# Kernel optimization log

Measured on AMD Instinct MI355X. Metric: run time of the kernel, lower is better.

Reference implementation:

```python
import jax, jax.numpy as jnp
import numpy as np

NEG_SLOPE = 0.01  # nn.LeakyReLU default


def setup_inputs() -> dict:
    key = jax.random.key(0)
    k1, k2, k3, k4, k5 = jax.random.split(key, 5)
    SLI, FEAT, NODE = 8, 64, 20000
    N = SLI * NODE          # 160000 graph nodes
    E = 2_560_000           # avg degree 16
    OUT = 64
    inputs = jax.random.normal(k1, (SLI, FEAT, NODE), dtype=jnp.float32)
    src = jax.random.randint(k2, (E,), 0, N, dtype=jnp.int64)
    dst = jax.random.randint(k3, (E,), 0, N, dtype=jnp.int64)
    # GraphConv params (glorot-ish scale)
    W = jax.random.normal(k4, (FEAT, OUT), dtype=jnp.float32) / np.sqrt(FEAT)
    b = jnp.zeros((OUT,), dtype=jnp.float32)
    return {"inputs": inputs, "W": W, "b": b, "src": src, "dst": dst}


def reference(inputs, W, b, src, dst):
    # inputs: [sli, feat, node] -> [sli*node, feat]  (dropout is eval-mode identity)
    sli, feat, node = inputs.shape
    x = jnp.transpose(inputs, (0, 2, 1)).reshape(-1, feat)
    N = sli * node
    ones = jnp.ones(src.shape, dtype=x.dtype)
    deg_out = jax.ops.segment_sum(ones, src, num_segments=N)  # out-degree of src
    deg_in = jax.ops.segment_sum(ones, dst, num_segments=N)   # in-degree of dst
    norm_src = jnp.where(deg_out > 0, deg_out, 1.0) ** -0.5
    norm_dst = jnp.where(deg_in > 0, deg_in, 1.0) ** -0.5
    # norm='both': scale src feats, sum-aggregate over edges, scale dst
    h = x * norm_src[:, None]
    agg = jax.ops.segment_sum(h[src], dst, num_segments=N)    # [N, feat]
    agg = agg * norm_dst[:, None]
    out = agg @ W + b                                          # [N, out]
    out = jax.nn.leaky_relu(out, NEG_SLOPE)
    # [N, out] -> [sli, node, out] -> [sli, out, node]
    return jnp.transpose(out.reshape(sli, node, -1), (0, 2, 1))
```

## Files before the change

### kernel.cpp

```cpp
#include <hip/hip_runtime.h>
#include <hip/hip_bf16.h>

constexpr int SLI  = 8;
constexpr int FEAT = 64;
constexpr int NODE = 20000;
constexpr int NTOT = SLI * NODE;
constexpr int OUTF = 64;
constexpr int CAP  = 48;
constexpr int NB   = 313;
constexpr int BCAP = 8960;
constexpr int EPB  = 4096;
constexpr int NDST = NTOT / 256;

typedef __attribute__((ext_vector_type(8))) short bf16x8;
typedef __attribute__((ext_vector_type(4))) float f32x4;

static __device__ inline unsigned short f2bf(float x) {
    unsigned u = __float_as_uint(x);
    unsigned r = (u + 0x7fffu + ((u >> 16) & 1u)) >> 16;
    return (unsigned short)r;
}

__global__ __launch_bounds__(256) void k_part(const int* __restrict__ src,
                                              const int* __restrict__ dst,
                                              int* __restrict__ cursor_d,
                                              unsigned* __restrict__ bucket_d,
                                              int* __restrict__ cursor_s,
                                              unsigned short* __restrict__ bucket_s, int E) {
    __shared__ unsigned       svalD[EPB];
    __shared__ unsigned short sbktD[EPB];
    __shared__ unsigned       sS[EPB];
    __shared__ int histD[NB], loffD[NB], lcurD[NB], baseD[NB];
    __shared__ int histS[NB], loffS[NB], lcurS[NB], baseS[NB];
    __shared__ int goffD[64], goffS[64];
    int t  = threadIdx.x;
    int e0 = blockIdx.x * EPB;
    for (int i = t; i < NB; i += 256) { histD[i] = 0; histS[i] = 0; }
    __syncthreads();
    int myS[16], myD[16];
#pragma unroll
    for (int i = 0; i < 16; ++i) {
        int idx = e0 + i * 256 + t;
        if (idx < E) {
            myS[i] = src[idx];
            myD[i] = dst[idx];
            atomicAdd(&histD[myD[i] >> 9], 1);
            atomicAdd(&histS[myS[i] >> 9], 1);
        } else { myS[i] = -1; myD[i] = -1; }
    }
    __syncthreads();
    int wv = t >> 6, ln = t & 63;
    if (wv == 0) {
        int b0 = ln * 5, s = 0;
#pragma unroll
        for (int j = 0; j < 5; ++j) { int bb = b0 + j; if (bb < NB) s += histD[bb]; }
        int x = s;
        for (int off = 1; off < 64; off <<= 1) {
            int y = __shfl_up(x, off, 64);
            if (ln >= off) x += y;
        }
        goffD[ln] = x - s;
    } else if (wv == 1) {
        int b0 = ln * 5, s = 0;
#pragma unroll
        for (int j = 0; j < 5; ++j) { int bb = b0 + j; if (bb < NB) s += histS[bb]; }
        int x = s;
        for (int off = 1; off < 64; off <<= 1) {
            int y = __shfl_up(x, off, 64);
            if (ln >= off) x += y;
        }
        goffS[ln] = x - s;
    }
    __syncthreads();
    for (int bb = t; bb < NB; bb += 256) {
        int g5 = bb / 5;
        int sD = goffD[g5], sS2 = goffS[g5];
        for (int k = g5 * 5; k < bb; ++k) { sD += histD[k]; sS2 += histS[k]; }
        loffD[bb] = sD; lcurD[bb] = sD;
        baseD[bb] = atomicAdd(&cursor_d[bb], histD[bb]);
        loffS[bb] = sS2; lcurS[bb] = sS2;
        baseS[bb] = atomicAdd(&cursor_s[bb], histS[bb]);
    }
    __syncthreads();
#pragma unroll
    for (int i = 0; i < 16; ++i) {
        if (myD[i] >= 0) {
            int bD = myD[i] >> 9;
            int p  = atomicAdd(&lcurD[bD], 1);
            svalD[p] = ((unsigned)(myD[i] & 511) << 18) | (unsigned)myS[i];
            sbktD[p] = (unsigned short)bD;
            int bS = myS[i] >> 9;
            int q  = atomicAdd(&lcurS[bS], 1);
            sS[q] = ((unsigned)bS << 9) | (unsigned)(myS[i] & 511);
        }
    }
    __syncthreads();
    int nval = E - e0; if (nval > EPB) nval = EPB;
    for (int p = t; p < nval; p += 256) {
        int bD = sbktD[p];
        int wi = baseD[bD] + (p - loffD[bD]);
        if (wi < BCAP) bucket_d[(size_t)bD * BCAP + wi] = svalD[p];
        unsigned vs = sS[p];
        int bS = vs >> 9;
        int wj = baseS[bS] + (p - loffS[bS]);
        if (wj < BCAP) bucket_s[(size_t)bS * BCAP + wj] = (unsigned short)(vs & 511);
    }
}

__global__ __launch_bounds__(256) void k_fin(const int* __restrict__ cursor_d,
                                             const unsigned* __restrict__ bucket_d,
                                             const int* __restrict__ cursor_s,
                                             const unsigned short* __restrict__ bucket_s,
                                             int* __restrict__ col_ell,
                                             int* __restrict__ deg_in,
                                             int* __restrict__ deg_out) {
    __shared__ char lds[256 * CAP * 4 + 2048];
    int t = threadIdx.x;
    if (blockIdx.x < NDST) {
        int* ell = (int*)lds;
        int* cnt = (int*)(lds + 256 * CAP * 4);
        int blk  = blockIdx.x, b = blk >> 1, half = blk & 1;
        cnt[t] = 0;
        __syncthreads();
        int len = cursor_d[b]; if (len > BCAP) len = BCAP;
        const unsigned* p = bucket_d + (size_t)b * BCAP;
        for (int i = t; i < len; i += 256) {
            unsigned e = p[i];
            int dl = e >> 18;
            if ((dl >> 8) == half) {
                int r = dl & 255;
                int pos = atomicAdd(&cnt[r], 1);
                if (pos < CAP) ell[r * CAP + pos] = (int)(e & 0x3FFFFu);
            }
        }
        __syncthreads();
        int node0 = blk << 8;
        deg_in[node0 + t] = cnt[t];
        size_t gbase = (size_t)node0 * CAP;
        const int4* lsrc = (const int4*)ell;
        int4* gdst = (int4*)(col_ell + gbase);
#pragma unroll
        for (int i = 0; i < 12; ++i)
            gdst[i * 256 + t] = lsrc[i * 256 + t];
    } else {
        int* cnt = (int*)lds;
        int b = blockIdx.x - NDST;
        cnt[t] = 0; cnt[t + 256] = 0;
        __syncthreads();
        int len = cursor_s[b]; if (len > BCAP) len = BCAP;
        const unsigned short* p = bucket_s + (size_t)b * BCAP;
        for (int i = t; i < len; i += 256)
            atomicAdd(&cnt[p[i]], 1);
        __syncthreads();
        int n0 = b << 9;
        if (n0 + t < NTOT)       deg_out[n0 + t] = cnt[t];
        if (n0 + 256 + t < NTOT) deg_out[n0 + 256 + t] = cnt[t + 256];
    }
}

__global__ __launch_bounds__(256) void k_transpose(const float* __restrict__ in,
                                                   const int* __restrict__ deg_out,
                                                   unsigned short* __restrict__ xs) {
    __shared__ float tile[64][65];
    int sli = blockIdx.y;
    int n0  = blockIdx.x * 64;
    int t   = threadIdx.x;
    int fx  = t & 15;
    int fr  = t >> 4;
    const float* ip = in + (size_t)sli * FEAT * NODE;
    int nq = n0 + fx * 4;
#pragma unroll
    for (int i = 0; i < 4; ++i) {
        int f = fr + i * 16;
        float4 v = {0.f, 0.f, 0.f, 0.f};
        if (nq < NODE) v = *(const float4*)(ip + (size_t)f * NODE + nq);
        tile[f][fx * 4 + 0] = v.x;
        tile[f][fx * 4 + 1] = v.y;
        tile[f][fx * 4 + 2] = v.z;
        tile[f][fx * 4 + 3] = v.w;
    }
    __syncthreads();
    int h  = t & 31;
    int nr = t >> 5;
#pragma unroll
    for (int i = 0; i < 8; ++i) {
        int nl   = nr + i * 8;
        int node = n0 + nl;
        if (node < NODE) {
            int n = sli * NODE + node;
            int d = deg_out[n];
            float sc = rsqrtf(d > 0 ? (float)d : 1.f);
            unsigned lo = f2bf(tile[2 * h][nl] * sc);
            unsigned hi = f2bf(tile[2 * h + 1][nl] * sc);
            *(unsigned*)(xs + (size_t)n * 64 + 2 * h) = lo | (hi << 16);
        }
    }
}

__global__ __launch_bounds__(256) void k_agg_gemm(const int* __restrict__ deg_in,
                                                  const int* __restrict__ col_ell,
                                                  const unsigned short* __restrict__ xs,
                                                  const float* __restrict__ W,
                                                  const float* __restrict__ b,
                                                  float* __restrict__ out) {
    __shared__ char lds[18432];
    unsigned short* av = (unsigned short*)lds;
    unsigned short* wt = (unsigned short*)(lds + 9216);
    float (*otile)[65] = (float(*)[65])lds;

    int t    = threadIdx.x;
    int lane = t & 63;
    int w    = t >> 6;
    int g8   = lane >> 3;
    int f8   = lane & 7;
    int sli  = blockIdx.y;
    int n0   = blockIdx.x * 64;

#pragma unroll
    for (int i = 0; i < 16; ++i) {
        int idx = i * 256 + t;
        int f = idx >> 6, o = idx & 63;
        wt[o * 72 + f] = f2bf(W[idx]);
    }

    int m0 = w * 16;
    for (int ii = 0; ii < 16; ii += 2) {
        int rowA = m0 + ii, rowB = rowA + 1;
        int nodeA = n0 + rowA, nodeB = n0 + rowB;
        int nA = sli * NODE + nodeA, nB = sli * NODE + nodeB;
        int dA = (nodeA < NODE) ? deg_in[nA] : 0;
        int dB = (nodeB < NODE) ? deg_in[nB] : 0;
        int degA = dA < CAP ? dA : CAP;
        int degB = dB < CAP ? dB : CAP;
        int cA = (lane < degA) ? col_ell[(size_t)nA * CAP + lane] : NTOT;
        int cB = (lane < degB) ? col_ell[(size_t)nB * CAP + lane] : NTOT;
        float accA[8] = {0,0,0,0,0,0,0,0};
        float accB[8] = {0,0,0,0,0,0,0,0};
        int gmax = degA > degB ? degA : degB;
        int groups = (gmax + 7) >> 3;
        for (int j = 0; j < groups; ++j) {
            int idx = 8 * j + g8;
            int sA = __shfl(cA, idx, 64);
            int sB = __shfl(cB, idx, 64);
            uint4 vA = *(const uint4*)(xs + (size_t)sA * 64 + f8 * 8);
            uint4 vB = *(const uint4*)(xs + (size_t)sB * 64 + f8 * 8);
            accA[0] += __uint_as_float(vA.x << 16);
            accA[1] += __uint_as_float(vA.x & 0xffff0000u);
            accA[2] += __uint_as_float(vA.y << 16);
            accA[3] += __uint_as_float(vA.y & 0xffff0000u);
            accA[4] += __uint_as_float(vA.z << 16);
            accA[5] += __uint_as_float(vA.z & 0xffff0000u);
            accA[6] += __uint_as_float(vA.w << 16);
            accA[7] += __uint_as_float(vA.w & 0xffff0000u);
            accB[0] += __uint_as_float(vB.x << 16);
            accB[1] += __uint_as_float(vB.x & 0xffff0000u);
            accB[2] += __uint_as_float(vB.y << 16);
            accB[3] += __uint_as_float(vB.y & 0xffff0000u);
            accB[4] += __uint_as_float(vB.z << 16);
            accB[5] += __uint_as_float(vB.z & 0xffff0000u);
            accB[6] += __uint_as_float(vB.w << 16);
            accB[7] += __uint_as_float(vB.w & 0xffff0000u);
        }
#pragma unroll
        for (int k = 0; k < 8; ++k) {
            accA[k] += __shfl_xor(accA[k], 8, 64);
            accA[k] += __shfl_xor(accA[k], 16, 64);
            accA[k] += __shfl_xor(accA[k], 32, 64);
            accB[k] += __shfl_xor(accB[k], 8, 64);
            accB[k] += __shfl_xor(accB[k], 16, 64);
            accB[k] += __shfl_xor(accB[k], 32, 64);
        }
        if (g8 == 0) {
            float scA = rsqrtf(dA > 0 ? (float)dA : 1.f);
            float scB = rsqrtf(dB > 0 ? (float)dB : 1.f);
            uint4 hv;
            hv.x = (unsigned)f2bf(accA[0] * scA) | ((unsigned)f2bf(accA[1] * scA) << 16);
            hv.y = (unsigned)f2bf(accA[2] * scA) | ((unsigned)f2bf(accA[3] * scA) << 16);
            hv.z = (unsigned)f2bf(accA[4] * scA) | ((unsigned)f2bf(accA[5] * scA) << 16);
            hv.w = (unsigned)f2bf(accA[6] * scA) | ((unsigned)f2bf(accA[7] * scA) << 16);
            ((uint4*)(av + rowA * 72))[f8] = hv;
            hv.x = (unsigned)f2bf(accB[0] * scB) | ((unsigned)f2bf(accB[1] * scB) << 16);
            hv.y = (unsigned)f2bf(accB[2] * scB) | ((unsigned)f2bf(accB[3] * scB) << 16);
            hv.z = (unsigned)f2bf(accB[4] * scB) | ((unsigned)f2bf(accB[5] * scB) << 16);
            hv.w = (unsigned)f2bf(accB[6] * scB) | ((unsigned)f2bf(accB[7] * scB) << 16);
            ((uint4*)(av + rowB * 72))[f8] = hv;
        }
    }

    __syncthreads();

    int q = lane >> 4, r16 = lane & 15;
    bf16x8 afr[2], bfr[4][2];
#pragma unroll
    for (int ks = 0; ks < 2; ++ks)
        afr[ks] = *(const bf16x8*)(av + (m0 + r16) * 72 + ks * 32 + q * 8);
#pragma unroll
    for (int nt = 0; nt < 4; ++nt)
#pragma unroll
        for (int ks = 0; ks < 2; ++ks)
            bfr[nt][ks] = *(const bf16x8*)(wt + (nt * 16 + r16) * 72 + ks * 32 + q * 8);

    f32x4 acc4[4];
#pragma unroll
    for (int nt = 0; nt < 4; ++nt) acc4[nt] = (f32x4){0.f, 0.f, 0.f, 0.f};
#pragma unroll
    for (int nt = 0; nt < 4; ++nt)
#pragma unroll
        for (int ks = 0; ks < 2; ++ks)
            acc4[nt] = __builtin_amdgcn_mfma_f32_16x16x32_bf16(afr[ks], bfr[nt][ks], acc4[nt], 0, 0, 0);
    __syncthreads();

#pragma unroll
    for (int nt = 0; nt < 4; ++nt) {
        int oc = nt * 16 + r16;
        float bias = b[oc];
#pragma unroll
        for (int r = 0; r < 4; ++r) {
            float v = acc4[nt][r] + bias;
            v = v > 0.f ? v : 0.01f * v;
            otile[oc][m0 + q * 4 + r] = v;
        }
    }
    __syncthreads();

    const size_t obase = (size_t)sli * OUTF * NODE;
#pragma unroll
    for (int i = 0; i < 16; ++i) {
        int o    = w + i * 4;
        int node = n0 + lane;
        if (node < NODE)
            out[obase + (size_t)o * NODE + node] = otile[o][lane];
    }
}

extern "C" void kernel_launch(void* const* d_in, const int* in_sizes, int n_in,
                              void* d_out, int out_size, void* d_ws, size_t ws_size,
                              hipStream_t stream) {
    const float* inputs = (const float*)d_in[0];
    const float* W      = (const float*)d_in[1];
    const float* b      = (const float*)d_in[2];
    const int*   src    = (const int*)d_in[3];
    const int*   dst    = (const int*)d_in[4];
    float*       out    = (float*)d_out;
    const int E = in_sizes[3];

    char* ws = (char*)d_ws;
    int* deg_out = (int*)ws;
    int* deg_in  = (int*)(ws + (size_t)NTOT * 4);
    int* col_ell = (int*)(ws + (size_t)2 * NTOT * 4);
    char* R      = (char*)col_ell + (size_t)NTOT * CAP * 4;
    unsigned*       bucket_d = (unsigned*)R;
    unsigned short* bucket_s = (unsigned short*)(R + (size_t)NB * BCAP * 4);
    int*            cursors  = (int*)(R + (size_t)NB * BCAP * 6);
    int* cursor_d = cursors;
    int* cursor_s = cursors + NB;
    unsigned short* xs = (unsigned short*)R;

    hipMemsetAsync(cursors, 0, (size_t)2 * NB * 4, stream);
    hipMemsetAsync(xs + (size_t)NTOT * 64, 0, 64 * sizeof(unsigned short), stream);

    int PB = (E + EPB - 1) / EPB;
    k_part<<<PB, 256, 0, stream>>>(src, dst, cursor_d, bucket_d, cursor_s, bucket_s, E);

    k_fin<<<NDST + NB, 256, 0, stream>>>(cursor_d, bucket_d, cursor_s, bucket_s,
                                         col_ell, deg_in, deg_out);

    dim3 tgrid((NODE + 63) / 64, SLI);
    k_transpose<<<tgrid, 256, 0, stream>>>(inputs, deg_out, xs);

    k_agg_gemm<<<tgrid, 256, 0, stream>>>(deg_in, col_ell, xs, W, b, out);
}
```

Before: 242.0 us.

## Count out-degree with global atomics and gather four rows per pass

The out-degree computation no longer goes through a source-bucket partition and per-bucket LDS histogram. Instead k_part increments deg_out directly with global atomics, which removes the bucket_s writes and the extra k_fin blocks. The aggregation loop now processes four destination rows per iteration instead of two, so more independent gathers are in flight. The trade-off is millions of scattered global atomics and higher register pressure from the larger accumulator set.

```diff
diff --git a/kernel.cpp b/kernel.cpp
--- a/kernel.cpp
+++ b/kernel.cpp
@@ -25,17 +25,14 @@
                                               const int* __restrict__ dst,
                                               int* __restrict__ cursor_d,
                                               unsigned* __restrict__ bucket_d,
-                                              int* __restrict__ cursor_s,
-                                              unsigned short* __restrict__ bucket_s, int E) {
+                                              int* __restrict__ deg_out, int E) {
     __shared__ unsigned       svalD[EPB];
     __shared__ unsigned short sbktD[EPB];
-    __shared__ unsigned       sS[EPB];
     __shared__ int histD[NB], loffD[NB], lcurD[NB], baseD[NB];
-    __shared__ int histS[NB], loffS[NB], lcurS[NB], baseS[NB];
-    __shared__ int goffD[64], goffS[64];
+    __shared__ int goffD[64];
     int t  = threadIdx.x;
     int e0 = blockIdx.x * EPB;
-    for (int i = t; i < NB; i += 256) { histD[i] = 0; histS[i] = 0; }
+    for (int i = t; i < NB; i += 256) histD[i] = 0;
     __syncthreads();
     int myS[16], myD[16];
 #pragma unroll
@@ -45,7 +42,7 @@
             myS[i] = src[idx];
             myD[i] = dst[idx];
             atomicAdd(&histD[myD[i] >> 9], 1);
-            atomicAdd(&histS[myS[i] >> 9], 1);
+            atomicAdd(&deg_out[myS[i]], 1);
         } else { myS[i] = -1; myD[i] = -1; }
     }
     __syncthreads();
@@ -60,26 +57,14 @@
             if (ln >= off) x += y;
         }
         goffD[ln] = x - s;
-    } else if (wv == 1) {
-        int b0 = ln * 5, s = 0;
-#pragma unroll
-        for (int j = 0; j < 5; ++j) { int bb = b0 + j; if (bb < NB) s += histS[bb]; }
-        int x = s;
-        for (int off = 1; off < 64; off <<= 1) {
-            int y = __shfl_up(x, off, 64);
-            if (ln >= off) x += y;
-        }
-        goffS[ln] = x - s;
     }
     __syncthreads();
     for (int bb = t; bb < NB; bb += 256) {
         int g5 = bb / 5;
-        int sD = goffD[g5], sS2 = goffS[g5];
-        for (int k = g5 * 5; k < bb; ++k) { sD += histD[k]; sS2 += histS[k]; }
+        int sD = goffD[g5];
+        for (int k = g5 * 5; k < bb; ++k) sD += histD[k];
         loffD[bb] = sD; lcurD[bb] = sD;
         baseD[bb] = atomicAdd(&cursor_d[bb], histD[bb]);
-        loffS[bb] = sS2; lcurS[bb] = sS2;
-        baseS[bb] = atomicAdd(&cursor_s[bb], histS[bb]);
     }
     __syncthreads();
 #pragma unroll
@@ -89,9 +74,6 @@
             int p  = atomicAdd(&lcurD[bD], 1);
             svalD[p] = ((unsigned)(myD[i] & 511) << 18) | (unsigned)myS[i];
             sbktD[p] = (unsigned short)bD;
-            int bS = myS[i] >> 9;
-            int q  = atomicAdd(&lcurS[bS], 1);
-            sS[q] = ((unsigned)bS << 9) | (unsigned)(myS[i] & 511);
         }
     }
     __syncthreads();
@@ -100,62 +82,40 @@
         int bD = sbktD[p];
         int wi = baseD[bD] + (p - loffD[bD]);
         if (wi < BCAP) bucket_d[(size_t)bD * BCAP + wi] = svalD[p];
-        unsigned vs = sS[p];
-        int bS = vs >> 9;
-        int wj = baseS[bS] + (p - loffS[bS]);
-        if (wj < BCAP) bucket_s[(size_t)bS * BCAP + wj] = (unsigned short)(vs & 511);
     }
 }
 
 __global__ __launch_bounds__(256) void k_fin(const int* __restrict__ cursor_d,
                                              const unsigned* __restrict__ bucket_d,
-                                             const int* __restrict__ cursor_s,
-                                             const unsigned short* __restrict__ bucket_s,
                                              int* __restrict__ col_ell,
-                                             int* __restrict__ deg_in,
-                                             int* __restrict__ deg_out) {
-    __shared__ char lds[256 * CAP * 4 + 2048];
+                                             int* __restrict__ deg_in) {
+    __shared__ char lds[256 * CAP * 4 + 1024];
+    int* ell = (int*)lds;
+    int* cnt = (int*)(lds + 256 * CAP * 4);
     int t = threadIdx.x;
-    if (blockIdx.x < NDST) {
-        int* ell = (int*)lds;
-        int* cnt = (int*)(lds + 256 * CAP * 4);
-        int blk  = blockIdx.x, b = blk >> 1, half = blk & 1;
-        cnt[t] = 0;
-        __syncthreads();
-        int len = cursor_d[b]; if (len > BCAP) len = BCAP;
-        const unsigned* p = bucket_d + (size_t)b * BCAP;
-        for (int i = t; i < len; i += 256) {
-            unsigned e = p[i];
-            int dl = e >> 18;
-            if ((dl >> 8) == half) {
-                int r = dl & 255;
-                int pos = atomicAdd(&cnt[r], 1);
-                if (pos < CAP) ell[r * CAP + pos] = (int)(e & 0x3FFFFu);
-            }
-        }
-        __syncthreads();
-        int node0 = blk << 8;
-        deg_in[node0 + t] = cnt[t];
-        size_t gbase = (size_t)node0 * CAP;
-        const int4* lsrc = (const int4*)ell;
-        int4* gdst = (int4*)(col_ell + gbase);
-#pragma unroll
-        for (int i = 0; i < 12; ++i)
-            gdst[i * 256 + t] = lsrc[i * 256 + t];
-    } else {
-        int* cnt = (int*)lds;
-        int b = blockIdx.x - NDST;
-        cnt[t] = 0; cnt[t + 256] = 0;
-        __syncthreads();
-        int len = cursor_s[b]; if (len > BCAP) len = BCAP;
-        const unsigned short* p = bucket_s + (size_t)b * BCAP;
-        for (int i = t; i < len; i += 256)
-            atomicAdd(&cnt[p[i]], 1);
-        __syncthreads();
-        int n0 = b << 9;
-        if (n0 + t < NTOT)       deg_out[n0 + t] = cnt[t];
-        if (n0 + 256 + t < NTOT) deg_out[n0 + 256 + t] = cnt[t + 256];
-    }
+    int blk = blockIdx.x, b = blk >> 1, half = blk & 1;
+    cnt[t] = 0;
+    __syncthreads();
+    int len = cursor_d[b]; if (len > BCAP) len = BCAP;
+    const unsigned* p = bucket_d + (size_t)b * BCAP;
+    for (int i = t; i < len; i += 256) {
+        unsigned e = p[i];
+        int dl = e >> 18;
+        if ((dl >> 8) == half) {
+            int r = dl & 255;
+            int pos = atomicAdd(&cnt[r], 1);
+            if (pos < CAP) ell[r * CAP + pos] = (int)(e & 0x3FFFFu);
+        }
+    }
+    __syncthreads();
+    int node0 = blk << 8;
+    deg_in[node0 + t] = cnt[t];
+    size_t gbase = (size_t)node0 * CAP;
+    const int4* lsrc = (const int4*)ell;
+    int4* gdst = (int4*)(col_ell + gbase);
+#pragma unroll
+    for (int i = 0; i < 12; ++i)
+        gdst[i * 256 + t] = lsrc[i * 256 + t];
 }
 
 __global__ __launch_bounds__(256) void k_transpose(const float* __restrict__ in,
@@ -224,66 +184,65 @@
     }
 
     int m0 = w * 16;
-    for (int ii = 0; ii < 16; ii += 2) {
-        int rowA = m0 + ii, rowB = rowA + 1;
-        int nodeA = n0 + rowA, nodeB = n0 + rowB;
-        int nA = sli * NODE + nodeA, nB = sli * NODE + nodeB;
-        int dA = (nodeA < NODE) ? deg_in[nA] : 0;
-        int dB = (nodeB < NODE) ? deg_in[nB] : 0;
-        int degA = dA < CAP ? dA : CAP;
-        int degB = dB < CAP ? dB : CAP;
-        int cA = (lane < degA) ? col_ell[(size_t)nA * CAP + lane] : NTOT;
-        int cB = (lane < degB) ? col_ell[(size_t)nB * CAP + lane] : NTOT;
-        float accA[8] = {0,0,0,0,0,0,0,0};
-        float accB[8] = {0,0,0,0,0,0,0,0};
-        int gmax = degA > degB ? degA : degB;
+    for (int ii = 0; ii < 16; ii += 4) {
+        int dg[4], col[4];
+        int gmax = 0;
+#pragma unroll
+        for (int r = 0; r < 4; ++r) {
+            int node = n0 + m0 + ii + r;
+            int n    = sli * NODE + node;
+            int d    = (node < NODE) ? deg_in[n] : 0;
+            dg[r] = d;
+            int dc = d < CAP ? d : CAP;
+            if (dc > gmax) gmax = dc;
+            col[r] = (lane < dc) ? col_ell[(size_t)n * CAP + lane] : NTOT;
+        }
+        float acc[4][8];
+#pragma unroll
+        for (int r = 0; r < 4; ++r)
+#pragma unroll
+            for (int k = 0; k < 8; ++k) acc[r][k] = 0.f;
         int groups = (gmax + 7) >> 3;
+#pragma unroll 2
         for (int j = 0; j < groups; ++j) {
             int idx = 8 * j + g8;
-            int sA = __shfl(cA, idx, 64);
-            int sB = __shfl(cB, idx, 64);
-            uint4 vA = *(const uint4*)(xs + (size_t)sA * 64 + f8 * 8);
-            uint4 vB = *(const uint4*)(xs + (size_t)sB * 64 + f8 * 8);
-            accA[0] += __uint_as_float(vA.x << 16);
-            accA[1] += __uint_as_float(vA.x & 0xffff0000u);
-            accA[2] += __uint_as_float(vA.y << 16);
-            accA[3] += __uint_as_float(vA.y & 0xffff0000u);
-            accA[4] += __uint_as_float(vA.z << 16);
-            accA[5] += __uint_as_float(vA.z & 0xffff0000u);
-            accA[6] += __uint_as_float(vA.w << 16);
-            accA[7] += __uint_as_float(vA.w & 0xffff0000u);
-            accB[0] += __uint_as_float(vB.x << 16);
-            accB[1] += __uint_as_float(vB.x & 0xffff0000u);
-            accB[2] += __uint_as_float(vB.y << 16);
-            accB[3] += __uint_as_float(vB.y & 0xffff0000u);
-            accB[4] += __uint_as_float(vB.z << 16);
-            accB[5] += __uint_as_float(vB.z & 0xffff0000u);
-            accB[6] += __uint_as_float(vB.w << 16);
-            accB[7] += __uint_as_float(vB.w & 0xffff0000u);
-        }
-#pragma unroll
-        for (int k = 0; k < 8; ++k) {
-            accA[k] += __shfl_xor(accA[k], 8, 64);
-            accA[k] += __shfl_xor(accA[k], 16, 64);
-            accA[k] += __shfl_xor(accA[k], 32, 64);
-            accB[k] += __shfl_xor(accB[k], 8, 64);
-            accB[k] += __shfl_xor(accB[k], 16, 64);
-            accB[k] += __shfl_xor(accB[k], 32, 64);
-        }
+            uint4 v[4];
+#pragma unroll
+            for (int r = 0; r < 4; ++r) {
+                int s = __shfl(col[r], idx, 64);
+                v[r] = *(const uint4*)(xs + (size_t)s * 64 + f8 * 8);
+            }
+#pragma unroll
+            for (int r = 0; r < 4; ++r) {
+                acc[r][0] += __uint_as_float(v[r].x << 16);
+                acc[r][1] += __uint_as_float(v[r].x & 0xffff0000u);
+                acc[r][2] += __uint_as_float(v[r].y << 16);
+                acc[r][3] += __uint_as_float(v[r].y & 0xffff0000u);
+                acc[r][4] += __uint_as_float(v[r].z << 16);
+                acc[r][5] += __uint_as_float(v[r].z & 0xffff0000u);
+                acc[r][6] += __uint_as_float(v[r].w << 16);
+                acc[r][7] += __uint_as_float(v[r].w & 0xffff0000u);
+            }
+        }
+#pragma unroll
+        for (int r = 0; r < 4; ++r)
+#pragma unroll
+            for (int k = 0; k < 8; ++k) {
+                acc[r][k] += __shfl_xor(acc[r][k], 8, 64);
+                acc[r][k] += __shfl_xor(acc[r][k], 16, 64);
+                acc[r][k] += __shfl_xor(acc[r][k], 32, 64);
+            }
         if (g8 == 0) {
-            float scA = rsqrtf(dA > 0 ? (float)dA : 1.f);
-            float scB = rsqrtf(dB > 0 ? (float)dB : 1.f);
-            uint4 hv;
-            hv.x = (unsigned)f2bf(accA[0] * scA) | ((unsigned)f2bf(accA[1] * scA) << 16);
-            hv.y = (unsigned)f2bf(accA[2] * scA) | ((unsigned)f2bf(accA[3] * scA) << 16);
-            hv.z = (unsigned)f2bf(accA[4] * scA) | ((unsigned)f2bf(accA[5] * scA) << 16);
-            hv.w = (unsigned)f2bf(accA[6] * scA) | ((unsigned)f2bf(accA[7] * scA) << 16);
-            ((uint4*)(av + rowA * 72))[f8] = hv;
-            hv.x = (unsigned)f2bf(accB[0] * scB) | ((unsigned)f2bf(accB[1] * scB) << 16);
-            hv.y = (unsigned)f2bf(accB[2] * scB) | ((unsigned)f2bf(accB[3] * scB) << 16);
-            hv.z = (unsigned)f2bf(accB[4] * scB) | ((unsigned)f2bf(accB[5] * scB) << 16);
-            hv.w = (unsigned)f2bf(accB[6] * scB) | ((unsigned)f2bf(accB[7] * scB) << 16);
-            ((uint4*)(av + rowB * 72))[f8] = hv;
+#pragma unroll
+            for (int r = 0; r < 4; ++r) {
+                float sc = rsqrtf(dg[r] > 0 ? (float)dg[r] : 1.f);
+                uint4 hv;
+                hv.x = (unsigned)f2bf(acc[r][0] * sc) | ((unsigned)f2bf(acc[r][1] * sc) << 16);
+                hv.y = (unsigned)f2bf(acc[r][2] * sc) | ((unsigned)f2bf(acc[r][3] * sc) << 16);
+                hv.z = (unsigned)f2bf(acc[r][4] * sc) | ((unsigned)f2bf(acc[r][5] * sc) << 16);
+                hv.w = (unsigned)f2bf(acc[r][6] * sc) | ((unsigned)f2bf(acc[r][7] * sc) << 16);
+                ((uint4*)(av + (m0 + ii + r) * 72))[f8] = hv;
+            }
         }
     }
 
@@ -349,21 +308,18 @@
     int* deg_in  = (int*)(ws + (size_t)NTOT * 4);
     int* col_ell = (int*)(ws + (size_t)2 * NTOT * 4);
     char* R      = (char*)col_ell + (size_t)NTOT * CAP * 4;
-    unsigned*       bucket_d = (unsigned*)R;
-    unsigned short* bucket_s = (unsigned short*)(R + (size_t)NB * BCAP * 4);
-    int*            cursors  = (int*)(R + (size_t)NB * BCAP * 6);
-    int* cursor_d = cursors;
-    int* cursor_s = cursors + NB;
+    unsigned* bucket_d = (unsigned*)R;
+    int*      cursor_d = (int*)(R + (size_t)NB * BCAP * 4);
     unsigned short* xs = (unsigned short*)R;
 
-    hipMemsetAsync(cursors, 0, (size_t)2 * NB * 4, stream);
+    hipMemsetAsync(cursor_d, 0, (size_t)NB * 4, stream);
+    hipMemsetAsync(deg_out, 0, (size_t)NTOT * 4, stream);
     hipMemsetAsync(xs + (size_t)NTOT * 64, 0, 64 * sizeof(unsigned short), stream);
 
     int PB = (E + EPB - 1) / EPB;
-    k_part<<<PB, 256, 0, stream>>>(src, dst, cursor_d, bucket_d, cursor_s, bucket_s, E);
-
-    k_fin<<<NDST + NB, 256, 0, stream>>>(cursor_d, bucket_d, cursor_s, bucket_s,
-                                         col_ell, deg_in, deg_out);
+    k_part<<<PB, 256, 0, stream>>>(src, dst, cursor_d, bucket_d, deg_out, E);
+
+    k_fin<<<NDST, 256, 0, stream>>>(cursor_d, bucket_d, col_ell, deg_in);
 
     dim3 tgrid((NODE + 63) / 64, SLI);
     k_transpose<<<tgrid, 256, 0, stream>>>(inputs, deg_out, xs);
```

After: 323.1 us. 33.5% more time.
